# Kernel optimization log

Measured on AMD Instinct MI355X. Metric: run time of the kernel, lower is better.

The kernel has to match this reference:

```python
import jax, jax.numpy as jnp
import numpy as np

# Static config (must match init_kwargs)
IMG_H, IMG_W = 48, 160
BEV_H, BEV_W = 128, 128
X_MIN, X_MAX, Y_MIN, Y_MAX = -51.2, 51.2, -51.2, 51.2
RES_X = (X_MAX - X_MIN) / BEV_W
RES_Y = (Y_MAX - Y_MIN) / BEV_H
C, D, B = 128, 64, 2


def setup_inputs() -> dict:
    key = jax.random.key(0)
    k1, k2, k3, k4 = jax.random.split(key, 4)
    img_features = jax.random.normal(k1, (B, C, IMG_H, IMG_W), dtype=jnp.float32)
    # depth distribution per pixel (softmax over D, as a depth net would emit)
    depth_probs = jax.nn.softmax(jax.random.normal(k2, (B, D, IMG_H, IMG_W), dtype=jnp.float32), axis=1)
    # depth bin centers: 1m .. 60m
    depth_values = jnp.linspace(1.0, 60.0, D, dtype=jnp.float32)
    # realistic pinhole intrinsics (feature-map scale) with tiny per-cam jitter
    fx, fy, cx, cy = 120.0, 120.0, IMG_W / 2.0, IMG_H / 2.0
    K0 = jnp.array([[fx, 0.0, cx], [0.0, fy, cy], [0.0, 0.0, 1.0]], dtype=jnp.float32)
    K = K0[None] + 0.01 * jax.random.normal(k3, (B, 3, 3), dtype=jnp.float32) * jnp.array(
        [[1.0, 0.0, 1.0], [0.0, 1.0, 1.0], [0.0, 0.0, 0.0]], dtype=jnp.float32)
    # cam->lidar extrinsic: cam z (forward) -> lidar x, cam x -> -lidar y, cam y -> -lidar z
    R0 = jnp.array([[0.0, 0.0, 1.0], [-1.0, 0.0, 0.0], [0.0, -1.0, 0.0]], dtype=jnp.float32)
    t0 = jnp.array([1.5, 0.0, 1.8], dtype=jnp.float32)
    T0 = jnp.eye(4, dtype=jnp.float32).at[:3, :3].set(R0).at[:3, 3].set(t0)
    T = T0[None] + jnp.zeros((B, 4, 4), dtype=jnp.float32)
    T = T.at[:, :3, 3].add(0.05 * jax.random.normal(k4, (B, 3), dtype=jnp.float32))
    return {"img_features": img_features, "depth_probs": depth_probs,
            "depth_values": depth_values, "K": K, "T": T}


def _lss_forward(img_features, depth_probs, depth_values, K, T):
    Bn, Cn, H, W = img_features.shape
    Dn = depth_values.shape[0]
    # homogeneous pixel grid [H, W, 3]
    gx, gy = jnp.meshgrid(jnp.arange(W, dtype=jnp.float32),
                          jnp.arange(H, dtype=jnp.float32), indexing="xy")
    grid = jnp.stack([gx, gy, jnp.ones_like(gx)], axis=-1)
    # unproject: rays [B, H, W, 3]
    K_inv = jnp.linalg.inv(K)
    rays = jnp.einsum("bij,hwj->bhwi", K_inv, grid)
    # points in camera frame [B, D, H, W, 3]
    pts_cam = depth_values[None, :, None, None, None] * rays[:, None]
    # camera -> lidar
    pts = jnp.einsum("bij,bdhwj->bdhwi", T[:, :3, :3], pts_cam) + T[:, None, None, None, :3, 3]
    x, y, z = pts[..., 0], pts[..., 1], pts[..., 2]
    # torch .long() truncates toward zero -> astype int32 matches
    bx = ((x - X_MIN) / RES_X).astype(jnp.int32)
    by = ((y - Y_MIN) / RES_Y).astype(jnp.int32)
    valid = (bx >= 0) & (bx < BEV_W) & (by >= 0) & (by < BEV_H) & (z > 0)
    # depth-weighted features [B, D, H, W, C], masked instead of gathered
    weighted = jnp.einsum("bchw,bdhw->bdhwc", img_features, depth_probs)
    weighted = weighted * valid[..., None]
    idx = jnp.where(valid, by * BEV_W + bx, 0).reshape(Bn, -1)
    feats = weighted.reshape(Bn, -1, Cn)
    bev_flat = jax.vmap(lambda f, i: jax.ops.segment_sum(f, i, num_segments=BEV_H * BEV_W))(feats, idx)
    return bev_flat.reshape(Bn, BEV_H, BEV_W, Cn).transpose(0, 3, 1, 2)


def reference(img_features, depth_probs, depth_values, K, T):
    return _lss_forward(img_features, depth_probs, depth_values, K, T)
```

## Files before the change

### kernel.cpp

```cpp
#include <hip/hip_runtime.h>

constexpr int IMG_H = 48, IMG_W = 160;
constexpr int HW    = IMG_H * IMG_W;
constexpr int BEV_H = 128, BEV_W = 128;
constexpr int NCELL = BEV_H * BEV_W;
constexpr int C_DIM = 128, D_DIM = 64, B_DIM = 2;
constexpr int NCELL_TOT = B_DIM * NCELL;
constexpr int NPIX_TOT  = B_DIM * HW;
constexpr int NPTS      = NPIX_TOT * D_DIM;
constexpr int MAX_ENTRIES = NPTS;
constexpr int CHUNK = 64;
constexpr int NSHARD = 16;
constexpr float X_MIN = -51.2f, Y_MIN = -51.2f;
constexpr float RES_X = 102.4f / 128.0f;
constexpr float RES_Y = 102.4f / 128.0f;

typedef _Float16 half2v __attribute__((ext_vector_type(2)));

constexpr size_t WS_IMG_T = 0;
constexpr size_t WS_IMG_T_WORDS = (size_t)B_DIM * HW * C_DIM / 2;
constexpr size_t WS_HIST2 = WS_IMG_T + WS_IMG_T_WORDS;
constexpr size_t WS_OUT_T = WS_HIST2 + (size_t)NSHARD * NCELL_TOT;
constexpr size_t WS_HIST  = WS_OUT_T + (size_t)NCELL_TOT * C_DIM;
constexpr size_t WS_OFFS  = WS_HIST + NCELL_TOT;
constexpr size_t WS_EKEY  = WS_OFFS + NCELL_TOT + 4;
constexpr size_t WS_EW16  = WS_EKEY + MAX_ENTRIES;
constexpr size_t WS_NEED_CM = (WS_EW16 + MAX_ENTRIES / 2) * 4;

__device__ inline int point_shard(int tid) {
    return ((tid >> 2) + (tid >> 8)) & (NSHARD - 1);
}

__device__ inline void make_ray(const float* __restrict__ K, int b, float gx, float gy,
                                float& rx, float& ry, float& rz) {
    const float* Kb = K + b * 9;
    const float a00 = Kb[0], a01 = Kb[1], a02 = Kb[2];
    const float a10 = Kb[3], a11 = Kb[4], a12 = Kb[5];
    const float a20 = Kb[6], a21 = Kb[7], a22 = Kb[8];
    const float det = a00 * (a11 * a22 - a12 * a21)
                    - a01 * (a10 * a22 - a12 * a20)
                    + a02 * (a10 * a21 - a11 * a20);
    const float inv = 1.0f / det;
    const float i00 =  (a11 * a22 - a12 * a21) * inv;
    const float i01 = -(a01 * a22 - a02 * a21) * inv;
    const float i02 =  (a01 * a12 - a02 * a11) * inv;
    const float i10 = -(a10 * a22 - a12 * a20) * inv;
    const float i11 =  (a00 * a22 - a02 * a20) * inv;
    const float i12 = -(a00 * a12 - a02 * a10) * inv;
    const float i20 =  (a10 * a21 - a11 * a20) * inv;
    const float i21 = -(a00 * a21 - a01 * a20) * inv;
    const float i22 =  (a00 * a11 - a01 * a10) * inv;
    rx = i00 * gx + i01 * gy + i02;
    ry = i10 * gx + i11 * gy + i12;
    rz = i20 * gx + i21 * gy + i22;
}

__device__ inline int point_gcell(int tid, const float* __restrict__ dv,
                                  const float* __restrict__ K,
                                  const float* __restrict__ T) {
    const int pix = tid % HW;
    const int bd  = tid / HW;
    const int d   = bd % D_DIM;
    const int b   = bd / D_DIM;
    const int h = pix / IMG_W, w = pix % IMG_W;
    float rx, ry, rz;
    make_ray(K, b, (float)w, (float)h, rx, ry, rz);
    const float* Tb = T + b * 16;
    const float dep = dv[d];
    const float px = dep * rx, py = dep * ry, pz = dep * rz;
    const float x = Tb[0] * px + Tb[1] * py + Tb[2]  * pz + Tb[3];
    const float y = Tb[4] * px + Tb[5] * py + Tb[6]  * pz + Tb[7];
    const float z = Tb[8] * px + Tb[9] * py + Tb[10] * pz + Tb[11];
    const int bx = (int)((x - X_MIN) / RES_X);
    const int by = (int)((y - Y_MIN) / RES_Y);
    const bool valid = (bx >= 0) && (bx < BEV_W) && (by >= 0) && (by < BEV_H) && (z > 0.0f);
    return valid ? (b * NCELL + by * BEV_W + bx) : -1;
}

__device__ inline bool wave_runs(int gcell, int lane, int& run_len, int& leader_idx) {
    const int left = __shfl_up(gcell, 1);
    const bool is_leader = (lane == 0) || (left != gcell);
    const unsigned long long lmask = __ballot(is_leader);
    const unsigned long long rest = (lane == 63) ? 0ULL : (lmask >> (lane + 1));
    const int f = __ffsll((unsigned long long)rest);
    run_len = f ? f : (64 - lane);
    const unsigned long long below =
        lmask & ((lane == 63) ? ~0ULL : ((1ULL << (lane + 1)) - 1ULL));
    leader_idx = 63 - __clzll((long long)below);
    return is_leader;
}

__global__ __launch_bounds__(256) void k_transpose(const float* __restrict__ img,
                                                   _Float16* __restrict__ img_t) {
    __shared__ float tile[32][33];
    const int b = blockIdx.z;
    const int tx = threadIdx.x, ty = threadIdx.y;
    const int pix0 = blockIdx.x * 32, c0 = blockIdx.y * 32;
    #pragma unroll
    for (int j = 0; j < 32; j += 8)
        tile[ty + j][tx] = img[((size_t)(b * C_DIM + c0 + ty + j)) * HW + pix0 + tx];
    __syncthreads();
    #pragma unroll
    for (int j = 0; j < 32; j += 8)
        img_t[((size_t)(b * HW + pix0 + ty + j)) * C_DIM + c0 + tx] =
            (_Float16)tile[tx][ty + j];
}

__global__ __launch_bounds__(256) void k_count(const float* __restrict__ dv,
                                               const float* __restrict__ K,
                                               const float* __restrict__ T,
                                               int* __restrict__ hist2) {
    const int tid = blockIdx.x * 256 + threadIdx.x;
    const int gcell = point_gcell(tid, dv, K, T);
    const int lane = threadIdx.x & 63;
    int run_len, leader_idx;
    const bool lead = wave_runs(gcell, lane, run_len, leader_idx);
    if (lead && gcell >= 0)
        atomicAdd(&hist2[(size_t)point_shard(tid) * NCELL_TOT + gcell], run_len);
}

__global__ __launch_bounds__(256) void k_reduce(const int* __restrict__ hist2,
                                                int* __restrict__ hist) {
    const int cell = blockIdx.x * 256 + threadIdx.x;
    int s = 0;
    #pragma unroll
    for (int sh = 0; sh < NSHARD; ++sh)
        s += hist2[(size_t)sh * NCELL_TOT + cell];
    hist[cell] = s;
}

__global__ __launch_bounds__(1024) void k_scan(const int* __restrict__ hist,
                                               int* __restrict__ offs) {
    __shared__ int lds[1024];
    const int t = threadIdx.x;
    int h[32];
    int s = 0;
    const int base = t * 32;
    #pragma unroll
    for (int k = 0; k < 32; ++k) { h[k] = hist[base + k]; s += h[k]; }
    lds[t] = s;
    __syncthreads();
    for (int off = 1; off < 1024; off <<= 1) {
        int v = (t >= off) ? lds[t - off] : 0;
        __syncthreads();
        lds[t] += v;
        __syncthreads();
    }
    int run = lds[t] - s;
    #pragma unroll
    for (int k = 0; k < 32; ++k) {
        offs[base + k] = run;
        run += h[k];
    }
    if (t == 1023) offs[NCELL_TOT] = lds[1023];
}

__global__ __launch_bounds__(256) void k_shardbase(int* __restrict__ hist2,
                                                   const int* __restrict__ offs) {
    const int cell = blockIdx.x * 256 + threadIdx.x;
    int run = offs[cell];
    #pragma unroll
    for (int sh = 0; sh < NSHARD; ++sh) {
        const size_t idx = (size_t)sh * NCELL_TOT + cell;
        const int cnt = hist2[idx];
        hist2[idx] = run;
        run += cnt;
    }
}

__global__ __launch_bounds__(256) void k_fill(const float* __restrict__ dp,
                                              const float* __restrict__ dv,
                                              const float* __restrict__ K,
                                              const float* __restrict__ T,
                                              int* __restrict__ cursor2,
                                              int* __restrict__ ekey,
                                              unsigned short* __restrict__ ew16) {
    const int tid = blockIdx.x * 256 + threadIdx.x;
    const int gcell = point_gcell(tid, dv, K, T);
    const int lane = threadIdx.x & 63;
    int run_len, leader_idx;
    const bool lead = wave_runs(gcell, lane, run_len, leader_idx);
    int base = 0;
    if (lead && gcell >= 0)
        base = atomicAdd(&cursor2[(size_t)point_shard(tid) * NCELL_TOT + gcell], run_len);
    base = __shfl(base, leader_idx);
    if (gcell < 0) return;
    const int slot = base + (lane - leader_idx);
    const float p = dp[tid];
    ekey[slot] = (gcell << 13) | (tid % HW);
    ew16[slot] = (unsigned short)__float2uint_rn(p * 65535.0f);
}

template <bool CELL_MAJOR>
__global__ __launch_bounds__(64) void k_chunk_gather(
    const _Float16* __restrict__ img_t,
    const int* __restrict__ offs,
    const int* __restrict__ ekey,
    const unsigned short* __restrict__ ew16,
    float* __restrict__ acc_out)
{
    const int total = offs[NCELL_TOT];
    const int base = blockIdx.x * CHUNK;
    if (base >= total) return;

    __shared__ int   s_key[CHUNK];
    __shared__ float s_w[CHUNK];
    {
        const int i = threadIdx.x;
        const int idx = min(base + i, total - 1);
        s_key[i] = ekey[idx];
        s_w[i]   = (base + i < total) ? (float)ew16[base + i] * (1.0f / 65535.0f)
                                      : 0.0f;
    }
    __syncthreads();

    const int c2 = threadIdx.x * 2;
    int prev = s_key[0] >> 13;
    float2 acc = make_float2(0.0f, 0.0f);
    #pragma unroll 8
    for (int k = 0; k < CHUNK; ++k) {
        const int key = s_key[k];
        const float wgt = s_w[k];
        const int gcell = key >> 13;
        const int pix = key & 8191;
        const int b = gcell >> 14;
        const half2v hv = *reinterpret_cast<const half2v*>(
            &img_t[((size_t)(b * HW + pix)) * C_DIM + c2]);
        if (gcell != prev) {
            if (CELL_MAJOR) {
                float* o = &acc_out[(size_t)prev * C_DIM + c2];
                atomicAdd(o, acc.x);
                atomicAdd(o + 1, acc.y);
            } else {
                const int pb = prev >> 14, pc = prev & (NCELL - 1);
                float* o = &acc_out[((size_t)(pb * C_DIM + c2)) * NCELL + pc];
                atomicAdd(o, acc.x);
                atomicAdd(o + NCELL, acc.y);
            }
            acc = make_float2(0.0f, 0.0f);
            prev = gcell;
        }
        acc.x = fmaf((float)hv[0], wgt, acc.x);
        acc.y = fmaf((float)hv[1], wgt, acc.y);
    }
    if (CELL_MAJOR) {
        float* o = &acc_out[(size_t)prev * C_DIM + c2];
        atomicAdd(o, acc.x);
        atomicAdd(o + 1, acc.y);
    } else {
        const int pb = prev >> 14, pc = prev & (NCELL - 1);
        float* o = &acc_out[((size_t)(pb * C_DIM + c2)) * NCELL + pc];
        atomicAdd(o, acc.x);
        atomicAdd(o + NCELL, acc.y);
    }
}

__global__ __launch_bounds__(256) void k_untranspose(const float* __restrict__ out_t,
                                                     float* __restrict__ out) {
    __shared__ float tile[32][33];
    const int b = blockIdx.z;
    const int tx = threadIdx.x, ty = threadIdx.y;
    const int cell0 = blockIdx.x * 32, c0 = blockIdx.y * 32;
    const float* src = out_t + (size_t)b * NCELL * C_DIM;
    #pragma unroll
    for (int j = 0; j < 32; j += 8)
        tile[ty + j][tx] = src[((size_t)(cell0 + ty + j)) * C_DIM + c0 + tx];
    __syncthreads();
    #pragma unroll
    for (int j = 0; j < 32; j += 8)
        out[((size_t)(b * C_DIM + c0 + ty + j)) * NCELL + cell0 + tx] = tile[tx][ty + j];
}

extern "C" void kernel_launch(void* const* d_in, const int* in_sizes, int n_in,
                              void* d_out, int out_size, void* d_ws, size_t ws_size,
                              hipStream_t stream) {
    const float* img = (const float*)d_in[0];
    const float* dp  = (const float*)d_in[1];
    const float* dv  = (const float*)d_in[2];
    const float* K   = (const float*)d_in[3];
    const float* T   = (const float*)d_in[4];
    float* out = (float*)d_out;

    float* ws_f   = (float*)d_ws;
    _Float16* img_t = (_Float16*)d_ws;
    int*   hist2  = (int*)d_ws + WS_HIST2;
    float* out_t  = ws_f + WS_OUT_T;
    int*   hist   = (int*)d_ws + WS_HIST;
    int*   offs   = (int*)d_ws + WS_OFFS;
    int*   ekey   = (int*)d_ws + WS_EKEY;
    unsigned short* ew16 = (unsigned short*)((int*)d_ws + WS_EW16);

    const bool cell_major = (ws_size >= WS_NEED_CM);

    if (cell_major) {
        hipMemsetAsync(hist2, 0,
                       ((size_t)NSHARD * NCELL_TOT + (size_t)NCELL_TOT * C_DIM) * sizeof(int),
                       stream);
    } else {
        hipMemsetAsync(hist2, 0, (size_t)NSHARD * NCELL_TOT * sizeof(int), stream);
        hipMemsetAsync(out, 0, (size_t)out_size * sizeof(float), stream);
    }

    k_transpose<<<dim3(HW / 32, C_DIM / 32, B_DIM), dim3(32, 8), 0, stream>>>(img, img_t);
    k_count<<<NPTS / 256, 256, 0, stream>>>(dv, K, T, hist2);
    k_reduce<<<NCELL_TOT / 256, 256, 0, stream>>>(hist2, hist);
    k_scan<<<1, 1024, 0, stream>>>(hist, offs);
    k_shardbase<<<NCELL_TOT / 256, 256, 0, stream>>>(hist2, offs);
    k_fill<<<NPTS / 256, 256, 0, stream>>>(dp, dv, K, T, hist2, ekey, ew16);
    if (cell_major) {
        k_chunk_gather<true><<<MAX_ENTRIES / CHUNK, 64, 0, stream>>>(
            img_t, offs, ekey, ew16, out_t);
        k_untranspose<<<dim3(NCELL / 32, C_DIM / 32, B_DIM), dim3(32, 8), 0, stream>>>(
            out_t, out);
    } else {
        k_chunk_gather<false><<<MAX_ENTRIES / CHUNK, 64, 0, stream>>>(
            img_t, offs, ekey, ew16, out);
    }
}
```

Before: 164.8 us.

## Pack four waves per gather block, use shuffles, and double-buffer feature loads

The gather kernel now runs four independent 64-entry chunks per 256-thread block instead of one chunk per 64-thread block. Keys and weights stay in registers and are broadcast with wave shuffles, so the shared-memory staging and the __syncthreads are gone. Feature loads are issued in groups of eight and double-buffered, so the next group's loads are in flight while the current group accumulates. The batch index is now taken from key bits 27 and up rather than computed from the cell. The aim is more memory-level parallelism and less block launch overhead, at the cost of more registers and more shuffle instructions.

Measured after the change: 154.9 us. -6.0%, faster.

```diff
diff --git a/kernel.cpp b/kernel.cpp
--- a/kernel.cpp
+++ b/kernel.cpp
@@ -10,6 +10,7 @@
 constexpr int NPTS      = NPIX_TOT * D_DIM;
 constexpr int MAX_ENTRIES = NPTS;
 constexpr int CHUNK = 64;
+constexpr int WAVES_PER_BLK = 4;
 constexpr int NSHARD = 16;
 constexpr float X_MIN = -51.2f, Y_MIN = -51.2f;
 constexpr float RES_X = 102.4f / 128.0f;
@@ -192,7 +193,7 @@
 }
 
 template <bool CELL_MAJOR>
-__global__ __launch_bounds__(64) void k_chunk_gather(
+__global__ __launch_bounds__(256) void k_chunk_gather(
     const _Float16* __restrict__ img_t,
     const int* __restrict__ offs,
     const int* __restrict__ ekey,
@@ -200,59 +201,85 @@
     float* __restrict__ acc_out)
 {
     const int total = offs[NCELL_TOT];
-    const int base = blockIdx.x * CHUNK;
+    const int wave  = threadIdx.x >> 6;
+    const int lane  = threadIdx.x & 63;
+    const int base  = (blockIdx.x * WAVES_PER_BLK + wave) * CHUNK;
     if (base >= total) return;
 
-    __shared__ int   s_key[CHUNK];
-    __shared__ float s_w[CHUNK];
-    {
-        const int i = threadIdx.x;
-        const int idx = min(base + i, total - 1);
-        s_key[i] = ekey[idx];
-        s_w[i]   = (base + i < total) ? (float)ew16[base + i] * (1.0f / 65535.0f)
-                                      : 0.0f;
-    }
-    __syncthreads();
-
-    const int c2 = threadIdx.x * 2;
-    int prev = s_key[0] >> 13;
+    const int eidx = min(base + lane, total - 1);
+    const int   mykey = ekey[eidx];
+    const float myw   = (base + lane < total)
+                        ? (float)ew16[base + lane] * (1.0f / 65535.0f) : 0.0f;
+
+    const int c2 = lane * 2;
+    int prev = __shfl(mykey, 0) >> 13;
     float2 acc = make_float2(0.0f, 0.0f);
-    #pragma unroll 8
-    for (int k = 0; k < CHUNK; ++k) {
-        const int key = s_key[k];
-        const float wgt = s_w[k];
-        const int gcell = key >> 13;
-        const int pix = key & 8191;
-        const int b = gcell >> 14;
-        const half2v hv = *reinterpret_cast<const half2v*>(
-            &img_t[((size_t)(b * HW + pix)) * C_DIM + c2]);
-        if (gcell != prev) {
-            if (CELL_MAJOR) {
-                float* o = &acc_out[(size_t)prev * C_DIM + c2];
-                atomicAdd(o, acc.x);
-                atomicAdd(o + 1, acc.y);
-            } else {
-                const int pb = prev >> 14, pc = prev & (NCELL - 1);
-                float* o = &acc_out[((size_t)(pb * C_DIM + c2)) * NCELL + pc];
-                atomicAdd(o, acc.x);
-                atomicAdd(o + NCELL, acc.y);
-            }
-            acc = make_float2(0.0f, 0.0f);
-            prev = gcell;
-        }
-        acc.x = fmaf((float)hv[0], wgt, acc.x);
-        acc.y = fmaf((float)hv[1], wgt, acc.y);
-    }
-    if (CELL_MAJOR) {
-        float* o = &acc_out[(size_t)prev * C_DIM + c2];
-        atomicAdd(o, acc.x);
-        atomicAdd(o + 1, acc.y);
-    } else {
-        const int pb = prev >> 14, pc = prev & (NCELL - 1);
-        float* o = &acc_out[((size_t)(pb * C_DIM + c2)) * NCELL + pc];
-        atomicAdd(o, acc.x);
-        atomicAdd(o + NCELL, acc.y);
-    }
+
+#define LOADG(g, V)                                                              \
+    do {                                                                         \
+        _Pragma("unroll")                                                        \
+        for (int k = 0; k < 8; ++k) {                                            \
+            const int key = __shfl(mykey, (g) * 8 + k);                          \
+            const int pix = key & 8191;                                          \
+            const int bb  = key >> 27;                                           \
+            V[k] = *reinterpret_cast<const half2v*>(                             \
+                &img_t[((size_t)(bb * HW + pix)) * C_DIM + c2]);                 \
+        }                                                                        \
+    } while (0)
+
+#define FLUSHP(cell)                                                             \
+    do {                                                                         \
+        if (CELL_MAJOR) {                                                        \
+            float* o = &acc_out[(size_t)(cell) * C_DIM + c2];                    \
+            atomicAdd(o, acc.x);                                                 \
+            atomicAdd(o + 1, acc.y);                                             \
+        } else {                                                                 \
+            const int pb = (cell) >> 14, pc = (cell) & (NCELL - 1);              \
+            float* o = &acc_out[((size_t)(pb * C_DIM + c2)) * NCELL + pc];       \
+            atomicAdd(o, acc.x);                                                 \
+            atomicAdd(o + NCELL, acc.y);                                         \
+        }                                                                        \
+    } while (0)
+
+#define ACCG(g, V)                                                               \
+    do {                                                                         \
+        _Pragma("unroll")                                                        \
+        for (int k = 0; k < 8; ++k) {                                            \
+            const int   key = __shfl(mykey, (g) * 8 + k);                        \
+            const float wgt = __shfl(myw, (g) * 8 + k);                          \
+            const int gcell = key >> 13;                                         \
+            if (gcell != prev) {                        \
+                FLUSHP(prev);                                                    \
+                acc = make_float2(0.0f, 0.0f);                                   \
+                prev = gcell;                                                    \
+            }                                                                    \
+            acc.x = fmaf((float)V[k][0], wgt, acc.x);                            \
+            acc.y = fmaf((float)V[k][1], wgt, acc.y);                            \
+        }                                                                        \
+    } while (0)
+
+    half2v va[8], vb[8];
+    LOADG(0, va);
+    LOADG(1, vb);
+    ACCG(0, va);
+    LOADG(2, va);
+    ACCG(1, vb);
+    LOADG(3, vb);
+    ACCG(2, va);
+    LOADG(4, va);
+    ACCG(3, vb);
+    LOADG(5, vb);
+    ACCG(4, va);
+    LOADG(6, va);
+    ACCG(5, vb);
+    LOADG(7, vb);
+    ACCG(6, va);
+    ACCG(7, vb);
+    FLUSHP(prev);
+
+#undef LOADG
+#undef FLUSHP
+#undef ACCG
 }
 
 __global__ __launch_bounds__(256) void k_untranspose(const float* __restrict__ out_t,
@@ -307,13 +334,14 @@
     k_scan<<<1, 1024, 0, stream>>>(hist, offs);
     k_shardbase<<<NCELL_TOT / 256, 256, 0, stream>>>(hist2, offs);
     k_fill<<<NPTS / 256, 256, 0, stream>>>(dp, dv, K, T, hist2, ekey, ew16);
+    constexpr int GATHER_BLOCKS = MAX_ENTRIES / (CHUNK * WAVES_PER_BLK);
     if (cell_major) {
-        k_chunk_gather<true><<<MAX_ENTRIES / CHUNK, 64, 0, stream>>>(
+        k_chunk_gather<true><<<GATHER_BLOCKS, 256, 0, stream>>>(
             img_t, offs, ekey, ew16, out_t);
         k_untranspose<<<dim3(NCELL / 32, C_DIM / 32, B_DIM), dim3(32, 8), 0, stream>>>(
             out_t, out);
     } else {
-        k_chunk_gather<false><<<MAX_ENTRIES / CHUNK, 64, 0, stream>>>(
+        k_chunk_gather<false><<<GATHER_BLOCKS, 256, 0, stream>>>(
             img_t, offs, ekey, ew16, out);
     }
 }
```

## Replace sharded histogram and chunk gather with per-cell segment gather

Applied to the files above, without the earlier changes.

Drops the 16-way sharded histogram, the reduce kernel and the shard-base kernel, and fuses counting with the image transpose into one launch. The scan now emits a list of segments of up to 64 points per BEV cell. A new gather kernel processes one segment per wave, using readlane-broadcast keys and packed 32-bit pixel/weight entries, and writes directly when a cell fits in a single segment instead of using atomics. This cuts launches, atomics and metadata traffic, but relies on a single-block serial segment emission in the scan and on unsharded histogram atomics, which may contend more on hot cells.

Result: slower. 187.4 us (+13.7%).

```diff
diff --git a/kernel.cpp b/kernel.cpp
--- a/kernel.cpp
+++ b/kernel.cpp
@@ -8,28 +8,26 @@
 constexpr int NCELL_TOT = B_DIM * NCELL;
 constexpr int NPIX_TOT  = B_DIM * HW;
 constexpr int NPTS      = NPIX_TOT * D_DIM;
-constexpr int MAX_ENTRIES = NPTS;
-constexpr int CHUNK = 64;
-constexpr int NSHARD = 16;
+constexpr int SEGLEN    = 64;
+constexpr int MAX_SEGS  = NCELL_TOT + NPTS / SEGLEN;
+constexpr int CNT_BLOCKS = NPTS / 256;
+constexpr int TRN_BLOCKS = (HW / 32) * (C_DIM / 32) * B_DIM;
 constexpr float X_MIN = -51.2f, Y_MIN = -51.2f;
 constexpr float RES_X = 102.4f / 128.0f;
 constexpr float RES_Y = 102.4f / 128.0f;
 
 typedef _Float16 half2v __attribute__((ext_vector_type(2)));
 
-constexpr size_t WS_IMG_T = 0;
-constexpr size_t WS_IMG_T_WORDS = (size_t)B_DIM * HW * C_DIM / 2;
-constexpr size_t WS_HIST2 = WS_IMG_T + WS_IMG_T_WORDS;
-constexpr size_t WS_OUT_T = WS_HIST2 + (size_t)NSHARD * NCELL_TOT;
-constexpr size_t WS_HIST  = WS_OUT_T + (size_t)NCELL_TOT * C_DIM;
-constexpr size_t WS_OFFS  = WS_HIST + NCELL_TOT;
-constexpr size_t WS_EKEY  = WS_OFFS + NCELL_TOT + 4;
-constexpr size_t WS_EW16  = WS_EKEY + MAX_ENTRIES;
-constexpr size_t WS_NEED_CM = (WS_EW16 + MAX_ENTRIES / 2) * 4;
-
-__device__ inline int point_shard(int tid) {
-    return ((tid >> 2) + (tid >> 8)) & (NSHARD - 1);
-}
+constexpr size_t WS_IMG_T  = 0;
+constexpr size_t WS_SEGCNT = WS_IMG_T + (size_t)B_DIM * HW * C_DIM / 2;
+constexpr size_t WS_HIST   = WS_SEGCNT + 4;
+constexpr size_t WS_OUT_T  = WS_HIST + NCELL_TOT;
+constexpr size_t WS_OFFS   = WS_OUT_T + (size_t)NCELL_TOT * C_DIM;
+constexpr size_t WS_CURS   = WS_OFFS + NCELL_TOT;
+constexpr size_t WS_EPW    = WS_CURS + NCELL_TOT;
+constexpr size_t WS_SEGS   = WS_EPW + NPTS;
+constexpr size_t WS_TOTAL_WORDS = WS_SEGS + (size_t)MAX_SEGS * 2;
+constexpr size_t MEMSET_WORDS = 4 + NCELL_TOT + (size_t)NCELL_TOT * C_DIM;
 
 __device__ inline void make_ray(const float* __restrict__ K, int b, float gx, float gy,
                                 float& rx, float& ry, float& rz) {
@@ -90,47 +88,44 @@
     return is_leader;
 }
 
-__global__ __launch_bounds__(256) void k_transpose(const float* __restrict__ img,
-                                                   _Float16* __restrict__ img_t) {
+__global__ __launch_bounds__(256) void k_prep(const float* __restrict__ img,
+                                              _Float16* __restrict__ img_t,
+                                              const float* __restrict__ dv,
+                                              const float* __restrict__ K,
+                                              const float* __restrict__ T,
+                                              int* __restrict__ hist) {
     __shared__ float tile[32][33];
-    const int b = blockIdx.z;
-    const int tx = threadIdx.x, ty = threadIdx.y;
-    const int pix0 = blockIdx.x * 32, c0 = blockIdx.y * 32;
-    #pragma unroll
-    for (int j = 0; j < 32; j += 8)
-        tile[ty + j][tx] = img[((size_t)(b * C_DIM + c0 + ty + j)) * HW + pix0 + tx];
-    __syncthreads();
-    #pragma unroll
-    for (int j = 0; j < 32; j += 8)
-        img_t[((size_t)(b * HW + pix0 + ty + j)) * C_DIM + c0 + tx] =
-            (_Float16)tile[tx][ty + j];
-}
-
-__global__ __launch_bounds__(256) void k_count(const float* __restrict__ dv,
-                                               const float* __restrict__ K,
-                                               const float* __restrict__ T,
-                                               int* __restrict__ hist2) {
-    const int tid = blockIdx.x * 256 + threadIdx.x;
-    const int gcell = point_gcell(tid, dv, K, T);
-    const int lane = threadIdx.x & 63;
-    int run_len, leader_idx;
-    const bool lead = wave_runs(gcell, lane, run_len, leader_idx);
-    if (lead && gcell >= 0)
-        atomicAdd(&hist2[(size_t)point_shard(tid) * NCELL_TOT + gcell], run_len);
-}
-
-__global__ __launch_bounds__(256) void k_reduce(const int* __restrict__ hist2,
-                                                int* __restrict__ hist) {
-    const int cell = blockIdx.x * 256 + threadIdx.x;
-    int s = 0;
-    #pragma unroll
-    for (int sh = 0; sh < NSHARD; ++sh)
-        s += hist2[(size_t)sh * NCELL_TOT + cell];
-    hist[cell] = s;
+    if (blockIdx.x < CNT_BLOCKS) {
+        const int tid = blockIdx.x * 256 + threadIdx.x;
+        const int gcell = point_gcell(tid, dv, K, T);
+        const int lane = threadIdx.x & 63;
+        int run_len, leader_idx;
+        const bool lead = wave_runs(gcell, lane, run_len, leader_idx);
+        if (lead && gcell >= 0)
+            atomicAdd(&hist[gcell], run_len);
+    } else {
+        const int bi = blockIdx.x - CNT_BLOCKS;
+        const int px_t = bi % (HW / 32);
+        const int c_t  = (bi / (HW / 32)) % (C_DIM / 32);
+        const int b    = bi / ((HW / 32) * (C_DIM / 32));
+        const int tx = threadIdx.x & 31, ty = threadIdx.x >> 5;
+        const int pix0 = px_t * 32, c0 = c_t * 32;
+        #pragma unroll
+        for (int j = 0; j < 32; j += 8)
+            tile[ty + j][tx] = img[((size_t)(b * C_DIM + c0 + ty + j)) * HW + pix0 + tx];
+        __syncthreads();
+        #pragma unroll
+        for (int j = 0; j < 32; j += 8)
+            img_t[((size_t)(b * HW + pix0 + ty + j)) * C_DIM + c0 + tx] =
+                (_Float16)tile[tx][ty + j];
+    }
 }
 
 __global__ __launch_bounds__(1024) void k_scan(const int* __restrict__ hist,
-                                               int* __restrict__ offs) {
+                                               int* __restrict__ offs,
+                                               int* __restrict__ curs,
+                                               int* __restrict__ seg_cnt,
+                                               uint2* __restrict__ segs) {
     __shared__ int lds[1024];
     const int t = threadIdx.x;
     int h[32];
@@ -146,24 +141,28 @@
         lds[t] += v;
         __syncthreads();
     }
-    int run = lds[t] - s;
+    const int run0 = lds[t] - s;
+    int run = run0;
+    int nseg = 0;
     #pragma unroll
     for (int k = 0; k < 32; ++k) {
         offs[base + k] = run;
+        curs[base + k] = run;
         run += h[k];
-    }
-    if (t == 1023) offs[NCELL_TOT] = lds[1023];
-}
-
-__global__ __launch_bounds__(256) void k_shardbase(int* __restrict__ hist2,
-                                                   const int* __restrict__ offs) {
-    const int cell = blockIdx.x * 256 + threadIdx.x;
-    int run = offs[cell];
-    #pragma unroll
-    for (int sh = 0; sh < NSHARD; ++sh) {
-        const size_t idx = (size_t)sh * NCELL_TOT + cell;
-        const int cnt = hist2[idx];
-        hist2[idx] = run;
+        nseg += (h[k] + SEGLEN - 1) >> 6;
+    }
+    int sbase = atomicAdd(seg_cnt, nseg);
+    run = run0;
+    for (int k = 0; k < 32; ++k) {
+        const int cnt = h[k];
+        if (cnt > 0) {
+            const unsigned whole = (cnt <= SEGLEN) ? 1u : 0u;
+            for (int done = 0; done < cnt; done += SEGLEN) {
+                const unsigned len = (unsigned)min(SEGLEN, cnt - done);
+                segs[sbase++] = make_uint2((unsigned)(run + done),
+                                           (unsigned)(base + k) | (len << 15) | (whole << 22));
+            }
+        }
         run += cnt;
     }
 }
@@ -172,9 +171,8 @@
                                               const float* __restrict__ dv,
                                               const float* __restrict__ K,
                                               const float* __restrict__ T,
-                                              int* __restrict__ cursor2,
-                                              int* __restrict__ ekey,
-                                              unsigned short* __restrict__ ew16) {
+                                              int* __restrict__ curs,
+                                              unsigned* __restrict__ epw) {
     const int tid = blockIdx.x * 256 + threadIdx.x;
     const int gcell = point_gcell(tid, dv, K, T);
     const int lane = threadIdx.x & 63;
@@ -182,76 +180,86 @@
     const bool lead = wave_runs(gcell, lane, run_len, leader_idx);
     int base = 0;
     if (lead && gcell >= 0)
-        base = atomicAdd(&cursor2[(size_t)point_shard(tid) * NCELL_TOT + gcell], run_len);
+        base = atomicAdd(&curs[gcell], run_len);
     base = __shfl(base, leader_idx);
     if (gcell < 0) return;
     const int slot = base + (lane - leader_idx);
     const float p = dp[tid];
-    ekey[slot] = (gcell << 13) | (tid % HW);
-    ew16[slot] = (unsigned short)__float2uint_rn(p * 65535.0f);
-}
-
-template <bool CELL_MAJOR>
-__global__ __launch_bounds__(64) void k_chunk_gather(
+    epw[slot] = (unsigned)(tid % HW) | (__float2uint_rn(p * 65535.0f) << 13);
+}
+
+__global__ __launch_bounds__(256) void k_seg_gather(
     const _Float16* __restrict__ img_t,
-    const int* __restrict__ offs,
-    const int* __restrict__ ekey,
-    const unsigned short* __restrict__ ew16,
-    float* __restrict__ acc_out)
+    const int* __restrict__ seg_cnt,
+    const uint2* __restrict__ segs,
+    const unsigned* __restrict__ epw,
+    float* __restrict__ out_t)
 {
-    const int total = offs[NCELL_TOT];
-    const int base = blockIdx.x * CHUNK;
-    if (base >= total) return;
-
-    __shared__ int   s_key[CHUNK];
-    __shared__ float s_w[CHUNK];
-    {
-        const int i = threadIdx.x;
-        const int idx = min(base + i, total - 1);
-        s_key[i] = ekey[idx];
-        s_w[i]   = (base + i < total) ? (float)ew16[base + i] * (1.0f / 65535.0f)
-                                      : 0.0f;
-    }
-    __syncthreads();
-
-    const int c2 = threadIdx.x * 2;
-    int prev = s_key[0] >> 13;
+    const int nseg = seg_cnt[0];
+    const int sidx = blockIdx.x * 4 + (threadIdx.x >> 6);
+    if (sidx >= nseg) return;
+    const int lane = threadIdx.x & 63;
+    const uint2 sg = segs[sidx];
+    const int start  = (int)sg.x;
+    const int gcell  = (int)(sg.y & 32767u);
+    const int len    = (int)((sg.y >> 15) & 127u);
+    const bool whole = (sg.y >> 22) & 1u;
+    const int bb = gcell >> 14;
+
+    unsigned pw = 0;
+    if (lane < len) pw = epw[start + lane];
+
+    const int c2 = lane * 2;
+    const _Float16* rowbase = img_t + ((size_t)bb * HW) * C_DIM + c2;
     float2 acc = make_float2(0.0f, 0.0f);
-    #pragma unroll 8
-    for (int k = 0; k < CHUNK; ++k) {
-        const int key = s_key[k];
-        const float wgt = s_w[k];
-        const int gcell = key >> 13;
-        const int pix = key & 8191;
-        const int b = gcell >> 14;
-        const half2v hv = *reinterpret_cast<const half2v*>(
-            &img_t[((size_t)(b * HW + pix)) * C_DIM + c2]);
-        if (gcell != prev) {
-            if (CELL_MAJOR) {
-                float* o = &acc_out[(size_t)prev * C_DIM + c2];
-                atomicAdd(o, acc.x);
-                atomicAdd(o + 1, acc.y);
-            } else {
-                const int pb = prev >> 14, pc = prev & (NCELL - 1);
-                float* o = &acc_out[((size_t)(pb * C_DIM + c2)) * NCELL + pc];
-                atomicAdd(o, acc.x);
-                atomicAdd(o + NCELL, acc.y);
-            }
-            acc = make_float2(0.0f, 0.0f);
-            prev = gcell;
+
+#define LOAD16(G, V)                                                             \
+    do {                                                                         \
+        _Pragma("unroll")                                                        \
+        for (int j = 0; j < 16; ++j) {                                           \
+            const unsigned sk =                                                  \
+                (unsigned)__builtin_amdgcn_readlane((int)pw, (G) * 16 + j);      \
+            V[j] = *reinterpret_cast<const half2v*>(                             \
+                rowbase + (size_t)(sk & 8191u) * C_DIM);                         \
+        }                                                                        \
+    } while (0)
+
+#define ACC16(G, V)                                                              \
+    do {                                                                         \
+        _Pragma("unroll")                                                        \
+        for (int j = 0; j < 16; ++j) {                                           \
+            const unsigned sk =                                                  \
+                (unsigned)__builtin_amdgcn_readlane((int)pw, (G) * 16 + j);      \
+            const float w = (float)(sk >> 13);                                   \
+            acc.x = fmaf((float)V[j][0], w, acc.x);                              \
+            acc.y = fmaf((float)V[j][1], w, acc.y);                              \
+        }                                                                        \
+    } while (0)
+
+    half2v va[16], vb[16];
+    LOAD16(0, va);
+    if (len > 16) LOAD16(1, vb);
+    ACC16(0, va);
+    if (len > 16) {
+        if (len > 32) LOAD16(2, va);
+        ACC16(1, vb);
+        if (len > 32) {
+            if (len > 48) LOAD16(3, vb);
+            ACC16(2, va);
+            if (len > 48) ACC16(3, vb);
         }
-        acc.x = fmaf((float)hv[0], wgt, acc.x);
-        acc.y = fmaf((float)hv[1], wgt, acc.y);
-    }
-    if (CELL_MAJOR) {
-        float* o = &acc_out[(size_t)prev * C_DIM + c2];
-        atomicAdd(o, acc.x);
-        atomicAdd(o + 1, acc.y);
+    }
+#undef LOAD16
+#undef ACC16
+
+    const float scale = 1.0f / 65535.0f;
+    const float2 res = make_float2(acc.x * scale, acc.y * scale);
+    float* o = &out_t[(size_t)gcell * C_DIM + c2];
+    if (whole) {
+        *reinterpret_cast<float2*>(o) = res;
     } else {
-        const int pb = prev >> 14, pc = prev & (NCELL - 1);
-        float* o = &acc_out[((size_t)(pb * C_DIM + c2)) * NCELL + pc];
-        atomicAdd(o, acc.x);
-        atomicAdd(o + NCELL, acc.y);
+        atomicAdd(o, res.x);
+        atomicAdd(o + 1, res.y);
     }
 }
 
@@ -281,39 +289,22 @@
     const float* T   = (const float*)d_in[4];
     float* out = (float*)d_out;
 
-    float* ws_f   = (float*)d_ws;
     _Float16* img_t = (_Float16*)d_ws;
-    int*   hist2  = (int*)d_ws + WS_HIST2;
-    float* out_t  = ws_f + WS_OUT_T;
-    int*   hist   = (int*)d_ws + WS_HIST;
-    int*   offs   = (int*)d_ws + WS_OFFS;
-    int*   ekey   = (int*)d_ws + WS_EKEY;
-    unsigned short* ew16 = (unsigned short*)((int*)d_ws + WS_EW16);
-
-    const bool cell_major = (ws_size >= WS_NEED_CM);
-
-    if (cell_major) {
-        hipMemsetAsync(hist2, 0,
-                       ((size_t)NSHARD * NCELL_TOT + (size_t)NCELL_TOT * C_DIM) * sizeof(int),
-                       stream);
-    } else {
-        hipMemsetAsync(hist2, 0, (size_t)NSHARD * NCELL_TOT * sizeof(int), stream);
-        hipMemsetAsync(out, 0, (size_t)out_size * sizeof(float), stream);
-    }
-
-    k_transpose<<<dim3(HW / 32, C_DIM / 32, B_DIM), dim3(32, 8), 0, stream>>>(img, img_t);
-    k_count<<<NPTS / 256, 256, 0, stream>>>(dv, K, T, hist2);
-    k_reduce<<<NCELL_TOT / 256, 256, 0, stream>>>(hist2, hist);
-    k_scan<<<1, 1024, 0, stream>>>(hist, offs);
-    k_shardbase<<<NCELL_TOT / 256, 256, 0, stream>>>(hist2, offs);
-    k_fill<<<NPTS / 256, 256, 0, stream>>>(dp, dv, K, T, hist2, ekey, ew16);
-    if (cell_major) {
-        k_chunk_gather<true><<<MAX_ENTRIES / CHUNK, 64, 0, stream>>>(
-            img_t, offs, ekey, ew16, out_t);
-        k_untranspose<<<dim3(NCELL / 32, C_DIM / 32, B_DIM), dim3(32, 8), 0, stream>>>(
-            out_t, out);
-    } else {
-        k_chunk_gather<false><<<MAX_ENTRIES / CHUNK, 64, 0, stream>>>(
-            img_t, offs, ekey, ew16, out);
-    }
-}
+    int*   seg_cnt = (int*)d_ws + WS_SEGCNT;
+    int*   hist    = (int*)d_ws + WS_HIST;
+    float* out_t   = (float*)d_ws + WS_OUT_T;
+    int*   offs    = (int*)d_ws + WS_OFFS;
+    int*   curs    = (int*)d_ws + WS_CURS;
+    unsigned* epw  = (unsigned*)((int*)d_ws + WS_EPW);
+    uint2* segs    = (uint2*)((int*)d_ws + WS_SEGS);
+    (void)offs; (void)ws_size;
+
+    hipMemsetAsync(seg_cnt, 0, MEMSET_WORDS * sizeof(int), stream);
+
+    k_prep<<<CNT_BLOCKS + TRN_BLOCKS, 256, 0, stream>>>(img, img_t, dv, K, T, hist);
+    k_scan<<<1, 1024, 0, stream>>>(hist, offs, curs, seg_cnt, segs);
+    k_fill<<<NPTS / 256, 256, 0, stream>>>(dp, dv, K, T, curs, epw);
+    k_seg_gather<<<MAX_SEGS / 4, 256, 0, stream>>>(img_t, seg_cnt, segs, epw, out_t);
+    k_untranspose<<<dim3(NCELL / 32, C_DIM / 32, B_DIM), dim3(32, 8), 0, stream>>>(
+        out_t, out);
+}
```
